# Kernel optimization log

Hardware: AMD Instinct MI355X
Metric: run time of the kernel (lower is better)

## Reference

```python
import jax, jax.numpy as jnp
import numpy as np

BETA = 0.25


def setup_inputs() -> dict:
    key = jax.random.key(0)
    k1, k2 = jax.random.split(key)
    latents = jax.random.normal(k1, (16, 4096, 256), dtype=jnp.float32)
    K = 1024
    # torch init: uniform(-1/K, 1/K)
    codebook = jax.random.uniform(k2, (K, 256), dtype=jnp.float32, minval=-1.0 / K, maxval=1.0 / K)
    return {"latents": latents, "codebook": codebook}


def reference(latents, codebook):
    D = codebook.shape[1]
    flat = latents.reshape(-1, D)  # [N, D]
    dist = (jnp.sum(flat * flat, axis=1, keepdims=True)
            + jnp.sum(codebook * codebook, axis=1)
            - 2.0 * jnp.matmul(flat, codebook.T))
    encoding_inds = jnp.argmin(dist, axis=1)  # [N]
    # gather nearest codebook vectors (equivalent to one-hot @ codebook)
    quantized = codebook[encoding_inds].reshape(latents.shape)
    commitment_loss = jnp.mean((jax.lax.stop_gradient(quantized) - latents) ** 2)
    embedding_loss = jnp.mean((quantized - jax.lax.stop_gradient(latents)) ** 2)
    vq_loss = commitment_loss * BETA + embedding_loss
    # straight-through estimator
    quantized_st = latents + jax.lax.stop_gradient(quantized - latents)
    return quantized_st, vq_loss
```

## Files before the change

kernel.cpp:

```cpp
#include <hip/hip_runtime.h>

typedef __attribute__((ext_vector_type(4))) float f32x4;
typedef __attribute__((ext_vector_type(2))) long i64x2;

#define SCALE 262144.0f
#define NEG2S -524288.0f
#define INV_S2 1.4551915228366852e-11f
#define OFFS35 34359738368.0f

static __device__ __forceinline__ unsigned umin2(unsigned a, unsigned b) { return a < b ? a : b; }

static __device__ __forceinline__ float dec_e4m3(unsigned b) {
  int e = (b >> 3) & 15, m = b & 7;
  float v = e ? ldexpf((float)(8 + m), e - 10) : ldexpf((float)m, -9);
  return (b & 0x80) ? -v : v;
}

__global__ void vq_prep(const float* __restrict__ cb,
                        float* __restrict__ norms,
                        unsigned char* __restrict__ cbh,
                        float* __restrict__ loss_out) {
  if (blockIdx.x == 0 && threadIdx.x == 0) *loss_out = 0.0f;
  const int lane = threadIdx.x & 63;
  const int code = (blockIdx.x * blockDim.x + threadIdx.x) >> 6;
  const f32x4 v = ((const f32x4*)(cb + (long)code * 256))[lane];
  unsigned w = __builtin_amdgcn_cvt_pk_fp8_f32(v[0] * SCALE, v[1] * SCALE, 0, false);
  w = __builtin_amdgcn_cvt_pk_fp8_f32(v[2] * SCALE, v[3] * SCALE, w, true);
  float n = 0.f;
#pragma unroll
  for (int j = 0; j < 4; ++j) {
    float d = dec_e4m3((w >> (8 * j)) & 0xFFu);
    n = __builtin_fmaf(d, d, n);
  }
  const int newpos = ((lane >> 1) & 3) * 64 + (lane >> 3) * 8 + (lane & 1) * 4;
  *(unsigned*)(cbh + (long)code * 256 + newpos) = w;
#pragma unroll
  for (int m = 1; m < 64; m <<= 1) n += __shfl_xor(n, m);
  if (lane == 0) norms[code] = n + OFFS35;
}

#define BM 128
#define DD 256
#define NTHR 512
#define NSUB 16

__global__ __launch_bounds__(NTHR, 4)
void vq_main(const float* __restrict__ X,
             const float* __restrict__ CB,
             const float* __restrict__ norms_g,
             const unsigned char* __restrict__ cbh,
             float* __restrict__ out,
             float* __restrict__ loss_out,
             float lscale) {
  __shared__ __attribute__((aligned(16))) unsigned char Eb[2 * 16384];
  __shared__ __attribute__((aligned(16))) unsigned char Xs[32768];
  __shared__ __attribute__((aligned(16))) float nrmLds[1024];
  __shared__ unsigned keys[BM];
  __shared__ float wsumX[8];
  __shared__ float wsumS[8];

  const int t = threadIdx.x;
  const int lane = t & 63;
  const int wave = t >> 6;
  const int wr = wave >> 1;
  const int wc = wave & 1;
  const int lo16 = lane & 15;
  const int hi = lane >> 4;
  const long rowBase = (long)blockIdx.x * BM;

  const char* cbB = (const char*)cbh;
  char* ebBase = (char*)Eb;
#define STAGE_E(ST, BUF)                                                                      \
  {                                                                                           \
    _Pragma("unroll") for (int c = 0; c < 2; ++c) {                                           \
      unsigned o = (unsigned)(wave * 2048 + c * 1024 + lane * 16);                            \
      unsigned src = o ^ ((((o >> 8) & 7u)) << 4);                                            \
      __builtin_amdgcn_global_load_lds(                                                       \
          (const __attribute__((address_space(1))) void*)(cbB + (unsigned)(ST)*16384u + src), \
          (__attribute__((address_space(3))) void*)(ebBase + (unsigned)(BUF)*16384u + wave * 2048 + c * 1024), \
          16, 0, 0);                                                                          \
    }                                                                                         \
  }

  STAGE_E(0, 0);

  nrmLds[t] = norms_g[t];
  nrmLds[t + 512] = norms_g[t + 512];
  if (t < BM) keys[t] = 0xFFFFFFFFu;

  float xn = 0.f;
  {
    const f32x4* xr = (const f32x4*)(X + (rowBase + wave * 16 + lo16) * DD);
    const unsigned row = (unsigned)(wave * 16 + lo16);
    const unsigned wbase = row * 256 + (unsigned)(hi * 64);
    const unsigned swz3 = (row & 7u) << 3;
#pragma unroll
    for (int ks = 0; ks < 8; ++ks) {
      f32x4 v0 = __builtin_nontemporal_load(xr + ks * 8 + hi * 2);
      f32x4 v1 = __builtin_nontemporal_load(xr + ks * 8 + hi * 2 + 1);
#pragma unroll
      for (int j = 0; j < 4; ++j) xn = __builtin_fmaf(v0[j], v0[j], xn);
#pragma unroll
      for (int j = 0; j < 4; ++j) xn = __builtin_fmaf(v1[j], v1[j], xn);
      unsigned w0 = __builtin_amdgcn_cvt_pk_fp8_f32(v0[0], v0[1], 0, false);
      w0 = __builtin_amdgcn_cvt_pk_fp8_f32(v0[2], v0[3], w0, true);
      unsigned w1 = __builtin_amdgcn_cvt_pk_fp8_f32(v1[0], v1[1], 0, false);
      w1 = __builtin_amdgcn_cvt_pk_fp8_f32(v1[2], v1[3], w1, true);
      *(long*)((char*)Xs + ((wbase + ks * 8) ^ swz3)) = (long)w0 | ((long)w1 << 32);
    }
  }
  __syncthreads();

  long a[2][8];
#pragma unroll
  for (int s = 0; s < 2; ++s) {
    const unsigned row = (unsigned)(wr * 32 + s * 16 + lo16);
    const unsigned rbase = row * 256 + (unsigned)(hi * 64);
    const unsigned swz3 = (row & 7u) << 3;
#pragma unroll
    for (int ks = 0; ks < 8; ++ks)
      a[s][ks] = *(const long*)((const char*)Xs + ((rbase + ks * 8) ^ swz3));
  }

  unsigned best[2][4];
#pragma unroll
  for (int s = 0; s < 2; ++s)
#pragma unroll
    for (int r = 0; r < 4; ++r) best[s][r] = 0xFFFFFFFFu;

  const unsigned swzl = (unsigned)((lo16 & 7) << 4);
  unsigned nbase[2];
#pragma unroll
  for (int n = 0; n < 2; ++n) nbase[n] = (unsigned)((wc * 32 + n * 16 + lo16) * 256) ^ swzl;
  const unsigned hi64 = (unsigned)(hi * 64);

  for (int st = 0; st < NSUB; ++st) {
    if (st + 1 < NSUB) {
      STAGE_E(st + 1, (st + 1) & 1);
      asm volatile("s_waitcnt vmcnt(2)" ::: "memory");
    } else {
      asm volatile("s_waitcnt vmcnt(0)" ::: "memory");
    }
    __builtin_amdgcn_s_barrier();
    __builtin_amdgcn_sched_barrier(0);

    const char* eb = ebBase + (st & 1) * 16384;
    f32x4 acc[2][2];
#pragma unroll
    for (int s = 0; s < 2; ++s)
#pragma unroll
      for (int n = 0; n < 2; ++n) {
        f32x4 z = {0.f, 0.f, 0.f, 0.f};
        acc[s][n] = z;
      }

#pragma unroll
    for (int ph = 0; ph < 2; ++ph) {
      const unsigned k0 = hi64 + (unsigned)(ph * 32);
      i64x2 b0a = *(const i64x2*)(eb + (nbase[0] ^ k0));
      i64x2 b1a = *(const i64x2*)(eb + (nbase[1] ^ k0));
      i64x2 b0b = *(const i64x2*)(eb + (nbase[0] ^ (k0 + 16)));
      i64x2 b1b = *(const i64x2*)(eb + (nbase[1] ^ (k0 + 16)));
      __builtin_amdgcn_sched_barrier(0);
      __builtin_amdgcn_s_barrier();
      asm volatile("s_waitcnt lgkmcnt(0)" ::: "memory");
      __builtin_amdgcn_sched_barrier(0);
      __builtin_amdgcn_s_setprio(1);
      const int kb = 4 * ph;
      acc[0][0] = __builtin_amdgcn_mfma_f32_16x16x32_fp8_fp8(a[0][kb], b0a.x, acc[0][0], 0, 0, 0);
      acc[1][0] = __builtin_amdgcn_mfma_f32_16x16x32_fp8_fp8(a[1][kb], b0a.x, acc[1][0], 0, 0, 0);
      acc[0][1] = __builtin_amdgcn_mfma_f32_16x16x32_fp8_fp8(a[0][kb], b1a.x, acc[0][1], 0, 0, 0);
      acc[1][1] = __builtin_amdgcn_mfma_f32_16x16x32_fp8_fp8(a[1][kb], b1a.x, acc[1][1], 0, 0, 0);
      acc[0][0] = __builtin_amdgcn_mfma_f32_16x16x32_fp8_fp8(a[0][kb + 1], b0a.y, acc[0][0], 0, 0, 0);
      acc[1][0] = __builtin_amdgcn_mfma_f32_16x16x32_fp8_fp8(a[1][kb + 1], b0a.y, acc[1][0], 0, 0, 0);
      acc[0][1] = __builtin_amdgcn_mfma_f32_16x16x32_fp8_fp8(a[0][kb + 1], b1a.y, acc[0][1], 0, 0, 0);
      acc[1][1] = __builtin_amdgcn_mfma_f32_16x16x32_fp8_fp8(a[1][kb + 1], b1a.y, acc[1][1], 0, 0, 0);
      acc[0][0] = __builtin_amdgcn_mfma_f32_16x16x32_fp8_fp8(a[0][kb + 2], b0b.x, acc[0][0], 0, 0, 0);
      acc[1][0] = __builtin_amdgcn_mfma_f32_16x16x32_fp8_fp8(a[1][kb + 2], b0b.x, acc[1][0], 0, 0, 0);
      acc[0][1] = __builtin_amdgcn_mfma_f32_16x16x32_fp8_fp8(a[0][kb + 2], b1b.x, acc[0][1], 0, 0, 0);
      acc[1][1] = __builtin_amdgcn_mfma_f32_16x16x32_fp8_fp8(a[1][kb + 2], b1b.x, acc[1][1], 0, 0, 0);
      acc[0][0] = __builtin_amdgcn_mfma_f32_16x16x32_fp8_fp8(a[0][kb + 3], b0b.y, acc[0][0], 0, 0, 0);
      acc[1][0] = __builtin_amdgcn_mfma_f32_16x16x32_fp8_fp8(a[1][kb + 3], b0b.y, acc[1][0], 0, 0, 0);
      acc[0][1] = __builtin_amdgcn_mfma_f32_16x16x32_fp8_fp8(a[0][kb + 3], b1b.y, acc[0][1], 0, 0, 0);
      acc[1][1] = __builtin_amdgcn_mfma_f32_16x16x32_fp8_fp8(a[1][kb + 3], b1b.y, acc[1][1], 0, 0, 0);
      __builtin_amdgcn_s_setprio(0);
      __builtin_amdgcn_sched_barrier(0);
    }

#pragma unroll
    for (int n = 0; n < 2; ++n) {
      float nf = nrmLds[st * 64 + wc * 32 + n * 16 + lo16];
      unsigned code = (unsigned)(st * 64 + wc * 32 + n * 16 + lo16);
#pragma unroll
      for (int s = 0; s < 2; ++s)
#pragma unroll
        for (int r = 0; r < 4; ++r) {
          float sv = __builtin_fmaf(NEG2S, acc[s][n][r], nf);
          best[s][r] = umin2(best[s][r], (__float_as_uint(sv) & 0xFFFFFC00u) | code);
        }
    }
  }

#pragma unroll
  for (int s = 0; s < 2; ++s)
#pragma unroll
    for (int r = 0; r < 4; ++r) {
#pragma unroll
      for (int msk = 1; msk < 16; msk <<= 1)
        best[s][r] = umin2(best[s][r], (unsigned)__shfl_xor((int)best[s][r], msk));
    }
  if (lo16 == 0) {
#pragma unroll
    for (int s = 0; s < 2; ++s)
#pragma unroll
      for (int r = 0; r < 4; ++r) {
        atomicMin(&keys[wr * 32 + s * 16 + hi * 4 + r], best[s][r]);
      }
  }

#pragma unroll
  for (int msk = 1; msk < 64; msk <<= 1) xn += __shfl_xor(xn, msk);
  if (lane == 0) wsumX[wave] = xn;

  __syncthreads();

  float sc = 0.f;
  if (t < BM) {
    unsigned e = keys[t];
    float sr = __uint_as_float((e & 0xFFFFFC00u) | 512u) - OFFS35;
    sc = sr * INV_S2;
  }
#pragma unroll
  for (int msk = 1; msk < 64; msk <<= 1) sc += __shfl_xor(sc, msk);
  if (lane == 0) wsumS[wave] = sc;

  {
    const f32x4* CBv = (const f32x4*)CB;
    f32x4* Og = (f32x4*)(out + rowBase * DD);
#pragma unroll 4
    for (int i = 0; i < 16; ++i) {
      int idx = t + NTHR * i;
      int row = idx >> 6, d4 = idx & 63;
      int code = (int)(keys[row] & 1023u);
      f32x4 e = CBv[code * 64 + d4];
      __builtin_nontemporal_store(e, Og + idx);
    }
  }

  __syncthreads();
  if (t == 0) {
    float tot = 0.f;
#pragma unroll
    for (int w = 0; w < 8; ++w) tot += wsumX[w] + wsumS[w];
    atomicAdd(loss_out, tot * lscale);
  }
}

extern "C" void kernel_launch(void* const* d_in, const int* in_sizes, int n_in,
                              void* d_out, int out_size, void* d_ws, size_t ws_size,
                              hipStream_t stream) {
  const float* X = (const float*)d_in[0];
  const float* CB = (const float*)d_in[1];
  float* out = (float*)d_out;

  const int ND = in_sizes[0];
  const int K = in_sizes[1] / DD;
  const int N = ND / DD;

  float* ws_norms = (float*)d_ws;
  unsigned char* ws_cb = (unsigned char*)((char*)d_ws + 4096);
  float* loss_out = out + (size_t)ND;

  vq_prep<<<K / 4, 256, 0, stream>>>(CB, ws_norms, ws_cb, loss_out);

  const float lscale = 1.25f / (float)ND;
  vq_main<<<N / BM, NTHR, 0, stream>>>(X, CB, ws_norms, ws_cb, out, loss_out, lscale);
}
```

Measured before the change: 53.50 us.

## Halve row tile, reuse codebook buffer for X staging, raise occupancy

The row tile drops from 128 to 64 and the launch bounds are raised to allow 8 blocks per CU. The separate X staging buffer is removed: X is staged in the second half of the codebook double buffer, with an extra barrier before that half is overwritten. Waves are re-tiled so four waves split the 64 codes of each sub-tile and two waves split the rows. Idle waves load the norms while the others convert X to FP8. The aim is more resident blocks and a smaller LDS footprint to hide latency, at the cost of staging the codebook twice as often and less B-operand reuse per wave.

```diff
diff --git a/kernel.cpp b/kernel.cpp
--- a/kernel.cpp
+++ b/kernel.cpp
@@ -39,12 +39,12 @@
   if (lane == 0) norms[code] = n + OFFS35;
 }
 
-#define BM 128
+#define BM 64
 #define DD 256
 #define NTHR 512
 #define NSUB 16
 
-__global__ __launch_bounds__(NTHR, 4)
+__global__ __launch_bounds__(NTHR, 8)
 void vq_main(const float* __restrict__ X,
              const float* __restrict__ CB,
              const float* __restrict__ norms_g,
@@ -53,23 +53,32 @@
              float* __restrict__ loss_out,
              float lscale) {
   __shared__ __attribute__((aligned(16))) unsigned char Eb[2 * 16384];
-  __shared__ __attribute__((aligned(16))) unsigned char Xs[32768];
   __shared__ __attribute__((aligned(16))) float nrmLds[1024];
   __shared__ unsigned keys[BM];
   __shared__ float wsumX[8];
-  __shared__ float wsumS[8];
 
   const int t = threadIdx.x;
   const int lane = t & 63;
   const int wave = t >> 6;
-  const int wr = wave >> 1;
-  const int wc = wave & 1;
+  const int wr = wave >> 2;
+  const int wq = wave & 3;
   const int lo16 = lane & 15;
   const int hi = lane >> 4;
   const long rowBase = (long)blockIdx.x * BM;
 
   const char* cbB = (const char*)cbh;
   char* ebBase = (char*)Eb;
+#define STAGE_E(ST, BUF)                                                                      \
+  {                                                                                           \
+    _Pragma("unroll") for (int c = 0; c < 2; ++c) {                                           \
+      unsigned o = (unsigned)(wave * 2048 + c * 1024 + lane * 16);                            \
+      unsigned src = o ^ ((((o >> 8) & 7u)) << 4);                                            \
+      __builtin_amdgcn_global_load_lds(                                                       \
+          (const __attribute__((address_space(1))) void*)(cbB + (unsigned)(ST)*16384u + src), \
+          (__builtin_amdgcn_global_load_lds, __attribute__((address_space(3))) void*)0, 16, 0, 0); \
+    }                                                                                         \
+  }
+#undef STAGE_E
 #define STAGE_E(ST, BUF)                                                                      \
   {                                                                                           \
     _Pragma("unroll") for (int c = 0; c < 2; ++c) {                                           \
@@ -84,15 +93,13 @@
 
   STAGE_E(0, 0);
 
-  nrmLds[t] = norms_g[t];
-  nrmLds[t + 512] = norms_g[t + 512];
   if (t < BM) keys[t] = 0xFFFFFFFFu;
 
   float xn = 0.f;
-  {
+  if (wave < 4) {
     const f32x4* xr = (const f32x4*)(X + (rowBase + wave * 16 + lo16) * DD);
     const unsigned row = (unsigned)(wave * 16 + lo16);
-    const unsigned wbase = row * 256 + (unsigned)(hi * 64);
+    const unsigned wbase = 16384u + row * 256 + (unsigned)(hi * 64);
     const unsigned swz3 = (row & 7u) << 3;
 #pragma unroll
     for (int ks = 0; ks < 8; ++ks) {
@@ -106,8 +113,14 @@
       w0 = __builtin_amdgcn_cvt_pk_fp8_f32(v0[2], v0[3], w0, true);
       unsigned w1 = __builtin_amdgcn_cvt_pk_fp8_f32(v1[0], v1[1], 0, false);
       w1 = __builtin_amdgcn_cvt_pk_fp8_f32(v1[2], v1[3], w1, true);
-      *(long*)((char*)Xs + ((wbase + ks * 8) ^ swz3)) = (long)w0 | ((long)w1 << 32);
-    }
+      *(long*)(ebBase + ((wbase + ks * 8) ^ swz3)) = (long)w0 | ((long)w1 << 32);
+    }
+  } else {
+    const int idx = t - 256;
+    nrmLds[idx] = norms_g[idx];
+    nrmLds[idx + 256] = norms_g[idx + 256];
+    nrmLds[idx + 512] = norms_g[idx + 512];
+    nrmLds[idx + 768] = norms_g[idx + 768];
   }
   __syncthreads();
 
@@ -115,12 +128,13 @@
 #pragma unroll
   for (int s = 0; s < 2; ++s) {
     const unsigned row = (unsigned)(wr * 32 + s * 16 + lo16);
-    const unsigned rbase = row * 256 + (unsigned)(hi * 64);
+    const unsigned rbase = 16384u + row * 256 + (unsigned)(hi * 64);
     const unsigned swz3 = (row & 7u) << 3;
 #pragma unroll
     for (int ks = 0; ks < 8; ++ks)
-      a[s][ks] = *(const long*)((const char*)Xs + ((rbase + ks * 8) ^ swz3));
-  }
+      a[s][ks] = *(const long*)((const char*)ebBase + ((rbase + ks * 8) ^ swz3));
+  }
+  __syncthreads();
 
   unsigned best[2][4];
 #pragma unroll
@@ -129,9 +143,7 @@
     for (int r = 0; r < 4; ++r) best[s][r] = 0xFFFFFFFFu;
 
   const unsigned swzl = (unsigned)((lo16 & 7) << 4);
-  unsigned nbase[2];
-#pragma unroll
-  for (int n = 0; n < 2; ++n) nbase[n] = (unsigned)((wc * 32 + n * 16 + lo16) * 256) ^ swzl;
+  const unsigned nbase = (unsigned)((wq * 16 + lo16) * 256) ^ swzl;
   const unsigned hi64 = (unsigned)(hi * 64);
 
   for (int st = 0; st < NSUB; ++st) {
@@ -145,57 +157,44 @@
     __builtin_amdgcn_sched_barrier(0);
 
     const char* eb = ebBase + (st & 1) * 16384;
-    f32x4 acc[2][2];
-#pragma unroll
-    for (int s = 0; s < 2; ++s)
-#pragma unroll
-      for (int n = 0; n < 2; ++n) {
-        f32x4 z = {0.f, 0.f, 0.f, 0.f};
-        acc[s][n] = z;
-      }
+    f32x4 acc[2];
+#pragma unroll
+    for (int s = 0; s < 2; ++s) {
+      f32x4 z = {0.f, 0.f, 0.f, 0.f};
+      acc[s] = z;
+    }
 
 #pragma unroll
     for (int ph = 0; ph < 2; ++ph) {
       const unsigned k0 = hi64 + (unsigned)(ph * 32);
-      i64x2 b0a = *(const i64x2*)(eb + (nbase[0] ^ k0));
-      i64x2 b1a = *(const i64x2*)(eb + (nbase[1] ^ k0));
-      i64x2 b0b = *(const i64x2*)(eb + (nbase[0] ^ (k0 + 16)));
-      i64x2 b1b = *(const i64x2*)(eb + (nbase[1] ^ (k0 + 16)));
+      i64x2 bA = *(const i64x2*)(eb + (nbase ^ k0));
+      i64x2 bB = *(const i64x2*)(eb + (nbase ^ (k0 + 16)));
       __builtin_amdgcn_sched_barrier(0);
       __builtin_amdgcn_s_barrier();
       asm volatile("s_waitcnt lgkmcnt(0)" ::: "memory");
       __builtin_amdgcn_sched_barrier(0);
       __builtin_amdgcn_s_setprio(1);
       const int kb = 4 * ph;
-      acc[0][0] = __builtin_amdgcn_mfma_f32_16x16x32_fp8_fp8(a[0][kb], b0a.x, acc[0][0], 0, 0, 0);
-      acc[1][0] = __builtin_amdgcn_mfma_f32_16x16x32_fp8_fp8(a[1][kb], b0a.x, acc[1][0], 0, 0, 0);
-      acc[0][1] = __builtin_amdgcn_mfma_f32_16x16x32_fp8_fp8(a[0][kb], b1a.x, acc[0][1], 0, 0, 0);
-      acc[1][1] = __builtin_amdgcn_mfma_f32_16x16x32_fp8_fp8(a[1][kb], b1a.x, acc[1][1], 0, 0, 0);
-      acc[0][0] = __builtin_amdgcn_mfma_f32_16x16x32_fp8_fp8(a[0][kb + 1], b0a.y, acc[0][0], 0, 0, 0);
-      acc[1][0] = __builtin_amdgcn_mfma_f32_16x16x32_fp8_fp8(a[1][kb + 1], b0a.y, acc[1][0], 0, 0, 0);
-      acc[0][1] = __builtin_amdgcn_mfma_f32_16x16x32_fp8_fp8(a[0][kb + 1], b1a.y, acc[0][1], 0, 0, 0);
-      acc[1][1] = __builtin_amdgcn_mfma_f32_16x16x32_fp8_fp8(a[1][kb + 1], b1a.y, acc[1][1], 0, 0, 0);
-      acc[0][0] = __builtin_amdgcn_mfma_f32_16x16x32_fp8_fp8(a[0][kb + 2], b0b.x, acc[0][0], 0, 0, 0);
-      acc[1][0] = __builtin_amdgcn_mfma_f32_16x16x32_fp8_fp8(a[1][kb + 2], b0b.x, acc[1][0], 0, 0, 0);
-      acc[0][1] = __builtin_amdgcn_mfma_f32_16x16x32_fp8_fp8(a[0][kb + 2], b1b.x, acc[0][1], 0, 0, 0);
-      acc[1][1] = __builtin_amdgcn_mfma_f32_16x16x32_fp8_fp8(a[1][kb + 2], b1b.x, acc[1][1], 0, 0, 0);
-      acc[0][0] = __builtin_amdgcn_mfma_f32_16x16x32_fp8_fp8(a[0][kb + 3], b0b.y, acc[0][0], 0, 0, 0);
-      acc[1][0] = __builtin_amdgcn_mfma_f32_16x16x32_fp8_fp8(a[1][kb + 3], b0b.y, acc[1][0], 0, 0, 0);
-      acc[0][1] = __builtin_amdgcn_mfma_f32_16x16x32_fp8_fp8(a[0][kb + 3], b1b.y, acc[0][1], 0, 0, 0);
-      acc[1][1] = __builtin_amdgcn_mfma_f32_16x16x32_fp8_fp8(a[1][kb + 3], b1b.y, acc[1][1], 0, 0, 0);
+      acc[0] = __builtin_amdgcn_mfma_f32_16x16x32_fp8_fp8(a[0][kb], bA.x, acc[0], 0, 0, 0);
+      acc[1] = __builtin_amdgcn_mfma_f32_16x16x32_fp8_fp8(a[1][kb], bA.x, acc[1], 0, 0, 0);
+      acc[0] = __builtin_amdgcn_mfma_f32_16x16x32_fp8_fp8(a[0][kb + 1], bA.y, acc[0], 0, 0, 0);
+      acc[1] = __builtin_amdgcn_mfma_f32_16x16x32_fp8_fp8(a[1][kb + 1], bA.y, acc[1], 0, 0, 0);
+      acc[0] = __builtin_amdgcn_mfma_f32_16x16x32_fp8_fp8(a[0][kb + 2], bB.x, acc[0], 0, 0, 0);
+      acc[1] = __builtin_amdgcn_mfma_f32_16x16x32_fp8_fp8(a[1][kb + 2], bB.x, acc[1], 0, 0, 0);
+      acc[0] = __builtin_amdgcn_mfma_f32_16x16x32_fp8_fp8(a[0][kb + 3], bB.y, acc[0], 0, 0, 0);
+      acc[1] = __builtin_amdgcn_mfma_f32_16x16x32_fp8_fp8(a[1][kb + 3], bB.y, acc[1], 0, 0, 0);
       __builtin_amdgcn_s_setprio(0);
       __builtin_amdgcn_sched_barrier(0);
     }
 
-#pragma unroll
-    for (int n = 0; n < 2; ++n) {
-      float nf = nrmLds[st * 64 + wc * 32 + n * 16 + lo16];
-      unsigned code = (unsigned)(st * 64 + wc * 32 + n * 16 + lo16);
+    {
+      const float nf = nrmLds[st * 64 + wq * 16 + lo16];
+      const unsigned code = (unsigned)(st * 64 + wq * 16 + lo16);
 #pragma unroll
       for (int s = 0; s < 2; ++s)
 #pragma unroll
         for (int r = 0; r < 4; ++r) {
-          float sv = __builtin_fmaf(NEG2S, acc[s][n][r], nf);
+          float sv = __builtin_fmaf(NEG2S, acc[s][r], nf);
           best[s][r] = umin2(best[s][r], (__float_as_uint(sv) & 0xFFFFFC00u) | code);
         }
     }
@@ -226,19 +225,17 @@
 
   float sc = 0.f;
   if (t < BM) {
-    unsigned e = keys[t];
-    float sr = __uint_as_float((e & 0xFFFFFC00u) | 512u) - OFFS35;
+    float sr = __uint_as_float((keys[t] & 0xFFFFFC00u) | 512u) - OFFS35;
     sc = sr * INV_S2;
   }
 #pragma unroll
   for (int msk = 1; msk < 64; msk <<= 1) sc += __shfl_xor(sc, msk);
-  if (lane == 0) wsumS[wave] = sc;
 
   {
     const f32x4* CBv = (const f32x4*)CB;
     f32x4* Og = (f32x4*)(out + rowBase * DD);
 #pragma unroll 4
-    for (int i = 0; i < 16; ++i) {
+    for (int i = 0; i < 8; ++i) {
       int idx = t + NTHR * i;
       int row = idx >> 6, d4 = idx & 63;
       int code = (int)(keys[row] & 1023u);
@@ -247,11 +244,10 @@
     }
   }
 
-  __syncthreads();
   if (t == 0) {
-    float tot = 0.f;
-#pragma unroll
-    for (int w = 0; w < 8; ++w) tot += wsumX[w] + wsumS[w];
+    float tot = sc;
+#pragma unroll
+    for (int w = 0; w < 8; ++w) tot += wsumX[w];
     atomicAdd(loss_out, tot * lscale);
   }
 }
```

Measured after the change: 129.3 us. 142% more time.

## Split codebook across two blocks per row tile and move gather to separate kernel

Applied to the files above, without the earlier changes.

The argmin kernel now launches two blocks per 128-row tile, each scanning half of the codebook. Partial results are merged with a global atomicMin into a key buffer initialized by the prep kernel. A new gather kernel reads the merged keys, writes the selected codebook rows, and accumulates the distance part of the loss. The aim is more parallelism and a shorter serial codebook loop per block. In exchange, each latent tile is loaded and converted twice, and there is an extra launch plus a global key round-trip.

```diff
diff --git a/kernel.cpp b/kernel.cpp
--- a/kernel.cpp
+++ b/kernel.cpp
@@ -19,10 +19,13 @@
 __global__ void vq_prep(const float* __restrict__ cb,
                         float* __restrict__ norms,
                         unsigned char* __restrict__ cbh,
+                        unsigned* __restrict__ gkeys,
                         float* __restrict__ loss_out) {
-  if (blockIdx.x == 0 && threadIdx.x == 0) *loss_out = 0.0f;
+  const int g = blockIdx.x * blockDim.x + threadIdx.x;
+  if (g == 0) *loss_out = 0.0f;
+  gkeys[g] = 0xFFFFFFFFu;
   const int lane = threadIdx.x & 63;
-  const int code = (blockIdx.x * blockDim.x + threadIdx.x) >> 6;
+  const int code = g >> 6;
   const f32x4 v = ((const f32x4*)(cb + (long)code * 256))[lane];
   unsigned w = __builtin_amdgcn_cvt_pk_fp8_f32(v[0] * SCALE, v[1] * SCALE, 0, false);
   w = __builtin_amdgcn_cvt_pk_fp8_f32(v[2] * SCALE, v[3] * SCALE, w, true);
@@ -42,22 +45,20 @@
 #define BM 128
 #define DD 256
 #define NTHR 512
-#define NSUB 16
+#define NSUB 8
 
 __global__ __launch_bounds__(NTHR, 4)
-void vq_main(const float* __restrict__ X,
-             const float* __restrict__ CB,
-             const float* __restrict__ norms_g,
-             const unsigned char* __restrict__ cbh,
-             float* __restrict__ out,
-             float* __restrict__ loss_out,
-             float lscale) {
+void vq_argmin(const float* __restrict__ X,
+               const float* __restrict__ norms_g,
+               const unsigned char* __restrict__ cbh,
+               unsigned* __restrict__ gkeys,
+               float* __restrict__ loss_out,
+               float lscale) {
   __shared__ __attribute__((aligned(16))) unsigned char Eb[2 * 16384];
   __shared__ __attribute__((aligned(16))) unsigned char Xs[32768];
-  __shared__ __attribute__((aligned(16))) float nrmLds[1024];
+  __shared__ __attribute__((aligned(16))) float nrmLds[512];
   __shared__ unsigned keys[BM];
   __shared__ float wsumX[8];
-  __shared__ float wsumS[8];
 
   const int t = threadIdx.x;
   const int lane = t & 63;
@@ -66,7 +67,12 @@
   const int wc = wave & 1;
   const int lo16 = lane & 15;
   const int hi = lane >> 4;
-  const long rowBase = (long)blockIdx.x * BM;
+
+  const int bid = blockIdx.x;
+  const int half = (bid >> 3) & 1;
+  const int rowBlk = (bid & 7) | ((bid >> 4) << 3);
+  const long rowBase = (long)rowBlk * BM;
+  const unsigned halfByte = (unsigned)half * 131072u;
 
   const char* cbB = (const char*)cbh;
   char* ebBase = (char*)Eb;
@@ -76,7 +82,7 @@
       unsigned o = (unsigned)(wave * 2048 + c * 1024 + lane * 16);                            \
       unsigned src = o ^ ((((o >> 8) & 7u)) << 4);                                            \
       __builtin_amdgcn_global_load_lds(                                                       \
-          (const __attribute__((address_space(1))) void*)(cbB + (unsigned)(ST)*16384u + src), \
+          (const __attribute__((address_space(1))) void*)(cbB + halfByte + (unsigned)(ST)*16384u + src), \
           (__attribute__((address_space(3))) void*)(ebBase + (unsigned)(BUF)*16384u + wave * 2048 + c * 1024), \
           16, 0, 0);                                                                          \
     }                                                                                         \
@@ -84,8 +90,7 @@
 
   STAGE_E(0, 0);
 
-  nrmLds[t] = norms_g[t];
-  nrmLds[t + 512] = norms_g[t + 512];
+  if (t < 512) nrmLds[t] = norms_g[half * 512 + t];
   if (t < BM) keys[t] = 0xFFFFFFFFu;
 
   float xn = 0.f;
@@ -190,7 +195,7 @@
 #pragma unroll
     for (int n = 0; n < 2; ++n) {
       float nf = nrmLds[st * 64 + wc * 32 + n * 16 + lo16];
-      unsigned code = (unsigned)(st * 64 + wc * 32 + n * 16 + lo16);
+      unsigned code = (unsigned)((half << 9) + st * 64 + wc * 32 + n * 16 + lo16);
 #pragma unroll
       for (int s = 0; s < 2; ++s)
 #pragma unroll
@@ -224,36 +229,48 @@
 
   __syncthreads();
 
+  if (t < BM) atomicMin(&gkeys[rowBase + t], keys[t]);
+  if (t == 0 && half == 0) {
+    float tot = 0.f;
+#pragma unroll
+    for (int w = 0; w < 8; ++w) tot += wsumX[w];
+    atomicAdd(loss_out, tot * lscale);
+  }
+}
+
+__global__ __launch_bounds__(256, 8)
+void vq_gather(const float* __restrict__ CB,
+               const unsigned* __restrict__ gkeys,
+               float* __restrict__ out,
+               float* __restrict__ loss_out,
+               float lscale) {
+  __shared__ int codeL[64];
+  const int t = threadIdx.x;
+  const int lane = t & 63;
+  const int wave = t >> 6;
+  const long rowBase = (long)blockIdx.x * 64;
+
   float sc = 0.f;
-  if (t < BM) {
-    unsigned e = keys[t];
+  if (t < 64) {
+    unsigned e = gkeys[rowBase + t];
+    codeL[t] = (int)(e & 1023u);
     float sr = __uint_as_float((e & 0xFFFFFC00u) | 512u) - OFFS35;
     sc = sr * INV_S2;
   }
 #pragma unroll
   for (int msk = 1; msk < 64; msk <<= 1) sc += __shfl_xor(sc, msk);
-  if (lane == 0) wsumS[wave] = sc;
-
-  {
-    const f32x4* CBv = (const f32x4*)CB;
-    f32x4* Og = (f32x4*)(out + rowBase * DD);
+  __syncthreads();
+
+  const f32x4* CBv = (const f32x4*)CB;
+  f32x4* Og = (f32x4*)(out + rowBase * 256);
 #pragma unroll 4
-    for (int i = 0; i < 16; ++i) {
-      int idx = t + NTHR * i;
-      int row = idx >> 6, d4 = idx & 63;
-      int code = (int)(keys[row] & 1023u);
-      f32x4 e = CBv[code * 64 + d4];
-      __builtin_nontemporal_store(e, Og + idx);
-    }
-  }
-
-  __syncthreads();
-  if (t == 0) {
-    float tot = 0.f;
-#pragma unroll
-    for (int w = 0; w < 8; ++w) tot += wsumX[w] + wsumS[w];
-    atomicAdd(loss_out, tot * lscale);
-  }
+  for (int rc = 0; rc < 16; ++rc) {
+    const int row = rc * 4 + wave;
+    const int code = codeL[row];
+    f32x4 e = CBv[code * 64 + lane];
+    __builtin_nontemporal_store(e, Og + row * 64 + lane);
+  }
+  if (t == 0) atomicAdd(loss_out, sc * lscale);
 }
 
 extern "C" void kernel_launch(void* const* d_in, const int* in_sizes, int n_in,
@@ -269,10 +286,12 @@
 
   float* ws_norms = (float*)d_ws;
   unsigned char* ws_cb = (unsigned char*)((char*)d_ws + 4096);
+  unsigned* ws_keys = (unsigned*)((char*)d_ws + 4096 + 262144);
   float* loss_out = out + (size_t)ND;
 
-  vq_prep<<<K / 4, 256, 0, stream>>>(CB, ws_norms, ws_cb, loss_out);
-
   const float lscale = 1.25f / (float)ND;
-  vq_main<<<N / BM, NTHR, 0, stream>>>(X, CB, ws_norms, ws_cb, out, loss_out, lscale);
-}
+
+  vq_prep<<<K / 4, 256, 0, stream>>>(CB, ws_norms, ws_cb, ws_keys, loss_out);
+  vq_argmin<<<(N / BM) * 2, NTHR, 0, stream>>>(X, ws_norms, ws_cb, ws_keys, loss_out, lscale);
+  vq_gather<<<N / 64, 256, 0, stream>>>(CB, ws_keys, out, loss_out, lscale);
+}
```

New measurement: 69.54 us. 30.0% more time.
